# Kernel optimization log

Measured on AMD Instinct MI355X. Metric: run time of the kernel, lower is better.

Reference implementation:

```python
import jax, jax.numpy as jnp
import numpy as np
import math

B, L, DIM, H = 2, 2048, 512, 8


def setup_inputs() -> dict:
    key = jax.random.key(0)
    ks = jax.random.split(key, 8)
    s = 0.02
    return {
        "x": jax.random.normal(ks[0], (B, L, DIM), dtype=jnp.float32),
        "Wq": jax.random.normal(ks[1], (DIM, DIM), dtype=jnp.float32) * s,
        "Wk": jax.random.normal(ks[2], (DIM, DIM), dtype=jnp.float32) * s,
        "Wv": jax.random.normal(ks[3], (DIM, DIM), dtype=jnp.float32) * s,
        "Wb": jax.random.normal(ks[4], (H, DIM), dtype=jnp.float32) * s,   # content_bias weight
        "mixing": jax.random.normal(ks[5], (H, DIM), dtype=jnp.float32) * 0.2,  # UNIFORM init, std=0.2
        "Wd": jax.random.normal(ks[6], (DIM, DIM), dtype=jnp.float32) * s,
        "bd": jax.random.normal(ks[7], (DIM,), dtype=jnp.float32) * s,
    }


def reference(x, Wq, Wk, Wv, Wb, mixing, Wd, bd):
    b, l, d = x.shape
    h = mixing.shape[0]
    dh = d // h
    q = x @ Wq.T                      # [B,L,D]
    k = x @ Wk.T                      # [B,S,D]
    v = (x @ Wv.T).reshape(b, l, h, dh).transpose(0, 2, 1, 3)  # [B,H,S,dh]
    # scores[b,h,l,s] = sum_d q[b,l,d] * mixing[h,d] * k[b,s,d]
    scores = jnp.einsum("bld,hd,bsd->bhls", q, mixing, k)
    # content bias: [B,S,H] -> broadcast over query positions as [B,H,1,S]
    cb = jnp.einsum("bsd,hd->bhs", x, Wb)
    scale = math.sqrt(d / h)  # attention_head_size = dim / num_heads
    scores = (scores + cb[:, :, None, :]) / scale
    probs = jax.nn.softmax(scores, axis=-1)   # dropout disabled (eval)
    ctx = jnp.einsum("bhls,bhsd->bhld", probs, v)  # [B,H,L,dh]
    ctx = ctx.transpose(0, 2, 1, 3).reshape(b, l, d)
    return ctx @ Wd.T + bd
```

## Files before the change

kernel.cpp:

```cpp
#include <hip/hip_runtime.h>

#define B_ 2
#define L_ 2048
#define D_ 512
#define H_ 8
#define S_ 2048

typedef __attribute__((ext_vector_type(8))) short short8;
typedef __attribute__((ext_vector_type(8))) unsigned short ushort8;
typedef __attribute__((ext_vector_type(4))) unsigned short ushort4v;
typedef __attribute__((ext_vector_type(4))) float f32x4;
typedef __attribute__((ext_vector_type(16))) float f32x16;
typedef __attribute__((ext_vector_type(4))) float float4v;

__device__ __forceinline__ unsigned short f2bf(float f) {
    unsigned u = __float_as_uint(f);
    u += 0x7FFF + ((u >> 16) & 1);
    return (unsigned short)(u >> 16);
}
__device__ __forceinline__ float bf2f(unsigned short s) {
    return __uint_as_float(((unsigned)s) << 16);
}
__device__ __forceinline__ int swap23(int x) {
    return (x & ~12) | ((x & 4) << 1) | ((x & 8) >> 1);
}
__device__ __forceinline__ void async16(void* lds, const void* g) {
    __builtin_amdgcn_global_load_lds(
        (const __attribute__((address_space(1))) void*)(g),
        (__attribute__((address_space(3))) void*)(lds), 16, 0, 0);
}

__global__ __launch_bounds__(256) void cvt_all(const float* __restrict__ x,
                                               const float* __restrict__ w0, const float* __restrict__ w1,
                                               const float* __restrict__ w2, const float* __restrict__ w3,
                                               unsigned short* __restrict__ xb,
                                               unsigned short* __restrict__ d0, unsigned short* __restrict__ d1,
                                               unsigned short* __restrict__ d2, unsigned short* __restrict__ d3) {
    int i = blockIdx.x * 256 + threadIdx.x;
    const float* s;
    unsigned short* d;
    int idx;
    if (i < 524288) { s = x; d = xb; idx = i; }
    else {
        int off = i - 524288;
        int wsel = off >> 16; idx = off & 65535;
        s = (wsel == 0) ? w0 : (wsel == 1) ? w1 : (wsel == 2) ? w2 : w3;
        d = (wsel == 0) ? d0 : (wsel == 1) ? d1 : (wsel == 2) ? d2 : d3;
    }
    float4v v = *(const float4v*)(s + (size_t)idx * 4);
    ushort4v o;
    o[0] = f2bf(v[0]); o[1] = f2bf(v[1]); o[2] = f2bf(v[2]); o[3] = f2bf(v[3]);
    *(ushort4v*)(d + (size_t)idx * 4) = o;
}

__global__ __launch_bounds__(256) void cb_kernel(const float* __restrict__ x,
                                                 const float* __restrict__ Wb,
                                                 float* __restrict__ cb) {
    const int tid = threadIdx.x, w = tid >> 6, lane = tid & 63;
    const int row = blockIdx.x * 4 + w;
    const int h = lane >> 3, seg = lane & 7;
    const float* xp = x + (size_t)row * 512 + seg * 64;
    const float* wp = Wb + (size_t)h * 512 + seg * 64;
    float acc = 0.f;
    #pragma unroll
    for (int j = 0; j < 16; ++j) {
        float4v xv = *(const float4v*)(xp + j * 4);
        float4v wv = *(const float4v*)(wp + j * 4);
        acc += xv[0] * wv[0] + xv[1] * wv[1] + xv[2] * wv[2] + xv[3] * wv[3];
    }
    acc += __shfl_xor(acc, 1);
    acc += __shfl_xor(acc, 2);
    acc += __shfl_xor(acc, 4);
    if (seg == 0) {
        int b = row >> 11, s = row & 2047;
        cb[((size_t)(b * H_ + h)) * S_ + s] = acc * 0.125f;
    }
}

__device__ __forceinline__ void gemm128_core(const unsigned short* __restrict__ Ap,
                                             const unsigned short* __restrict__ Bp,
                                             short* sA, short* sB, int tid, f32x4 c[4][4]) {
    const int w = tid >> 6, lane = tid & 63, quad = lane >> 4, l15 = lane & 15;
    const int wm = (w >> 1) * 64, wn = (w & 1) * 64;
    for (int kc = 0; kc < 8; ++kc) {
        __syncthreads();
        #pragma unroll
        for (int j = 0; j < 4; ++j) {
            int i = tid + j * 256;
            int row = i >> 3, seg = i & 7;
            *(ushort8*)&sA[row * 72 + seg * 8] = *(const ushort8*)(Ap + (size_t)row * 512 + kc * 64 + seg * 8);
            *(ushort8*)&sB[row * 72 + seg * 8] = *(const ushort8*)(Bp + (size_t)row * 512 + kc * 64 + seg * 8);
        }
        __syncthreads();
        #pragma unroll
        for (int ks = 0; ks < 2; ++ks) {
            short8 a[4], b[4];
            #pragma unroll
            for (int ii = 0; ii < 4; ++ii)
                a[ii] = *(const short8*)&sA[(wm + ii * 16 + l15) * 72 + ks * 32 + quad * 8];
            #pragma unroll
            for (int jj = 0; jj < 4; ++jj)
                b[jj] = *(const short8*)&sB[(wn + jj * 16 + l15) * 72 + ks * 32 + quad * 8];
            #pragma unroll
            for (int ii = 0; ii < 4; ++ii)
                #pragma unroll
                for (int jj = 0; jj < 4; ++jj)
                    c[ii][jj] = __builtin_amdgcn_mfma_f32_16x16x32_bf16(a[ii], b[jj], c[ii][jj], 0, 0, 0);
        }
    }
}

__global__ __launch_bounds__(256) void gemm_qkv(const unsigned short* __restrict__ xb,
                                                const unsigned short* __restrict__ Wqb,
                                                const unsigned short* __restrict__ Wkb,
                                                const unsigned short* __restrict__ Wvb,
                                                unsigned short* __restrict__ qb,
                                                unsigned short* __restrict__ kpack,
                                                unsigned short* __restrict__ vt) {
    __shared__ short sA[128 * 72];
    __shared__ short sB[128 * 72];
    const int m0 = blockIdx.x * 128, n0 = blockIdx.y * 128, z = blockIdx.z;
    const unsigned short* Bsel = (z == 0) ? Wqb : ((z == 1) ? Wkb : Wvb);
    f32x4 c[4][4];
    #pragma unroll
    for (int ii = 0; ii < 4; ++ii)
        #pragma unroll
        for (int jj = 0; jj < 4; ++jj) { f32x4 zv = {0.f, 0.f, 0.f, 0.f}; c[ii][jj] = zv; }
    gemm128_core(xb + (size_t)m0 * 512, Bsel + (size_t)n0 * 512, sA, sB, threadIdx.x, c);
    const int tid = threadIdx.x, w = tid >> 6, lane = tid & 63, quad = lane >> 4, l15 = lane & 15;
    const int wm = (w >> 1) * 64, wn = (w & 1) * 64;
    #pragma unroll
    for (int ii = 0; ii < 4; ++ii) {
        const int mb = m0 + wm + ii * 16 + quad * 4;
        const int bb = mb >> 11;
        if (z == 0) {
            #pragma unroll
            for (int jj = 0; jj < 4; ++jj) {
                int ncol = n0 + wn + jj * 16 + l15;
                #pragma unroll
                for (int r = 0; r < 4; ++r)
                    qb[(size_t)(mb + r) * 512 + ncol] = f2bf(c[ii][jj][r]);
            }
        } else if (z == 1) {
            #pragma unroll
            for (int jj = 0; jj < 4; ++jj) {
                int d = n0 + wn + jj * 16 + l15;
                int f = d >> 4, hid = (d >> 3) & 1, jq = d & 7;
                #pragma unroll
                for (int r = 0; r < 4; ++r) {
                    int s = (mb + r) & 2047;
                    int t = s >> 5, rr = swap23(s & 31);
                    kpack[(((size_t)(bb * 64 + t)) * 32 + f) * 512 + hid * 256 + rr * 8 + jq]
                        = f2bf(c[ii][jj][r]);
                }
            }
        } else {
            const int hh = (n0 + wn) >> 6;
            const int s = mb & 2047;
            #pragma unroll
            for (int jj = 0; jj < 4; ++jj) {
                int dh = jj * 16 + l15;
                ushort4v o;
                o[0] = f2bf(c[ii][jj][0]); o[1] = f2bf(c[ii][jj][1]);
                o[2] = f2bf(c[ii][jj][2]); o[3] = f2bf(c[ii][jj][3]);
                *(ushort4v*)(vt + (((size_t)(bb * H_ + hh) * 64 + dh) * S_ + s)) = o;
            }
        }
    }
}

__global__ __launch_bounds__(256) void gemm_out(const unsigned short* __restrict__ ctxb,
                                                const unsigned short* __restrict__ Wdb,
                                                const float* __restrict__ bd,
                                                float* __restrict__ out) {
    __shared__ short sA[128 * 72];
    __shared__ short sB[128 * 72];
    const int m0 = blockIdx.x * 128, n0 = blockIdx.y * 128;
    f32x4 c[4][4];
    #pragma unroll
    for (int ii = 0; ii < 4; ++ii)
        #pragma unroll
        for (int jj = 0; jj < 4; ++jj) { f32x4 zv = {0.f, 0.f, 0.f, 0.f}; c[ii][jj] = zv; }
    gemm128_core(ctxb + (size_t)m0 * 512, Wdb + (size_t)n0 * 512, sA, sB, threadIdx.x, c);
    const int tid = threadIdx.x, w = tid >> 6, lane = tid & 63, quad = lane >> 4, l15 = lane & 15;
    const int wm = (w >> 1) * 64, wn = (w & 1) * 64;
    #pragma unroll
    for (int ii = 0; ii < 4; ++ii) {
        const int mb = m0 + wm + ii * 16 + quad * 4;
        #pragma unroll
        for (int jj = 0; jj < 4; ++jj) {
            int ncol = n0 + wn + jj * 16 + l15;
            float bias = bd[ncol];
            #pragma unroll
            for (int r = 0; r < 4; ++r)
                out[(size_t)(mb + r) * 512 + ncol] = c[ii][jj][r] + bias;
        }
    }
}

__global__ __launch_bounds__(256, 2) void flash_attn(const unsigned short* __restrict__ qb,
                                                     const unsigned short* __restrict__ kpack,
                                                     const unsigned short* __restrict__ vt,
                                                     const float* __restrict__ cb_all,
                                                     const float* __restrict__ mixing,
                                                     _Float16* __restrict__ Opart,
                                                     float* __restrict__ lpart) {
    __shared__ short sK[4][8192];
    __shared__ short sV[2][2048];
    const int bid = blockIdx.x;
    const int half = bid & 1, b = (bid >> 1) & 1, h = (bid >> 2) & 7, qt = bid >> 5;
    const int tid = threadIdx.x, w = tid >> 6, lane = tid & 63;
    const int l31 = lane & 31, hi = lane >> 5;
    const int q0 = qt * 128 + w * 32;
    const unsigned short* kbase = kpack + ((size_t)(b * 64 + half * 32)) * 32 * 512;
    const unsigned short* vtb = vt + ((size_t)(b * H_ + h) * 64) * (size_t)S_;
    const float* cbp = cb_all + (size_t)(b * H_ + h) * S_ + half * 1024;
    const float* mixh = mixing + h * D_;

    short8 qf[32];
    {
        const unsigned short* qrow = qb + ((size_t)(b * L_) + q0 + l31) * D_ + hi * 8;
        #pragma unroll
        for (int i = 0; i < 32; ++i) {
            ushort8 qv = *(const ushort8*)(qrow + i * 16);
            float4v ma = *(const float4v*)(mixh + i * 16 + hi * 8);
            float4v mb = *(const float4v*)(mixh + i * 16 + hi * 8 + 4);
            short8 ov;
            ov[0] = (short)f2bf(bf2f(qv[0]) * ma[0]);
            ov[1] = (short)f2bf(bf2f(qv[1]) * ma[1]);
            ov[2] = (short)f2bf(bf2f(qv[2]) * ma[2]);
            ov[3] = (short)f2bf(bf2f(qv[3]) * ma[3]);
            ov[4] = (short)f2bf(bf2f(qv[4]) * mb[0]);
            ov[5] = (short)f2bf(bf2f(qv[5]) * mb[1]);
            ov[6] = (short)f2bf(bf2f(qv[6]) * mb[2]);
            ov[7] = (short)f2bf(bf2f(qv[7]) * mb[3]);
            qf[i] = ov;
        }
    }
    asm volatile("s_waitcnt vmcnt(0)" ::: "memory");

    f32x16 acco0, acco1;
    #pragma unroll
    for (int i = 0; i < 16; ++i) { acco0[i] = 0.f; acco1[i] = 0.f; }
    float lsum = 0.f;
    f32x16 accsA, accsB;

    auto stageK = [&](int p) {
        const char* src = (const char*)(kbase + (size_t)p * 8192);
        char* dst = (char*)&sK[p & 3][0];
        #pragma unroll
        for (int ii = 0; ii < 4; ++ii)
            async16(dst + w * 1024 + ii * 4096, src + w * 1024 + ii * 4096 + (size_t)lane * 16);
    };
    auto stageV = [&](int u) {
        const unsigned short* gv = vtb + ((size_t)((w >> 1) * 32 + l31)) * (size_t)S_
                                   + half * 1024 + u * 32 + (w & 1) * 16 + hi * 8;
        async16((char*)&sV[u & 1][0] + w * 1024, gv);
    };
    auto qk_chunk = [&](const short* buf, int qbase) {
        __builtin_amdgcn_s_setprio(1);
        #pragma unroll
        for (int f = 0; f < 16; ++f) {
            short8 a = *(const short8*)&buf[f * 512 + lane * 8];
            if (f & 1) accsB = __builtin_amdgcn_mfma_f32_32x32x16_bf16(a, qf[qbase + f], accsB, 0, 0, 0);
            else       accsA = __builtin_amdgcn_mfma_f32_32x32x16_bf16(a, qf[qbase + f], accsA, 0, 0, 0);
        }
        __builtin_amdgcn_s_setprio(0);
    };
    auto softmax_pv = [&](int t) {
        const int s0 = t * 32;
        float p[16];
        #pragma unroll
        for (int R = 0; R < 16; ++R) {
            const int cr = (R & 3) + 8 * (R >> 2);
            const int idx = s0 + cr - 4 * ((R >> 2) & 1);
            float cbA = cbp[idx];
            float cbB = cbp[idx + 8];
            float cbv = hi ? cbB : cbA;
            float pe = __expf((accsA[R] + accsB[R]) * 0.125f + cbv);
            p[R] = pe;
            lsum += pe;
        }
        union { unsigned int u[4]; short8 s8; } P0, P1;
        #pragma unroll
        for (int j = 0; j < 4; ++j) {
            P0.u[j] = __builtin_amdgcn_perm(__float_as_uint(p[2 * j + 1]) + 0x8000u,
                                            __float_as_uint(p[2 * j]) + 0x8000u, 0x07060302u);
            P1.u[j] = __builtin_amdgcn_perm(__float_as_uint(p[8 + 2 * j + 1]) + 0x8000u,
                                            __float_as_uint(p[8 + 2 * j]) + 0x8000u, 0x07060302u);
        }
        const short* vbuf = &sV[t & 1][0];
        short8 av00 = *(const short8*)&vbuf[0 * 512 + lane * 8];
        short8 av01 = *(const short8*)&vbuf[1 * 512 + lane * 8];
        short8 av10 = *(const short8*)&vbuf[2 * 512 + lane * 8];
        short8 av11 = *(const short8*)&vbuf[3 * 512 + lane * 8];
        __builtin_amdgcn_s_setprio(1);
        acco0 = __builtin_amdgcn_mfma_f32_32x32x16_bf16(av00, P0.s8, acco0, 0, 0, 0);
        acco0 = __builtin_amdgcn_mfma_f32_32x32x16_bf16(av01, P1.s8, acco0, 0, 0, 0);
        acco1 = __builtin_amdgcn_mfma_f32_32x32x16_bf16(av10, P0.s8, acco1, 0, 0, 0);
        acco1 = __builtin_amdgcn_mfma_f32_32x32x16_bf16(av11, P1.s8, acco1, 0, 0, 0);
        __builtin_amdgcn_s_setprio(0);
    };

    stageK(0); stageK(1); stageV(0); stageK(2);

    for (int t = 0; t < 31; ++t) {
        #pragma unroll
        for (int i = 0; i < 16; ++i) { accsA[i] = 0.f; accsB[i] = 0.f; }
        const short* be = &sK[(t & 1) << 1][0];
        const short* bo = &sK[((t & 1) << 1) | 1][0];
        asm volatile("s_waitcnt vmcnt(9)" ::: "memory");
        __builtin_amdgcn_s_barrier();
        stageK(2 * t + 3);
        qk_chunk(be, 0);
        asm volatile("s_waitcnt vmcnt(8)" ::: "memory");
        __builtin_amdgcn_s_barrier();
        stageV(t + 1);
        if (t < 30) stageK(2 * t + 4);
        qk_chunk(bo, 16);
        softmax_pv(t);
    }
    {
        #pragma unroll
        for (int i = 0; i < 16; ++i) { accsA[i] = 0.f; accsB[i] = 0.f; }
        asm volatile("s_waitcnt vmcnt(5)" ::: "memory");
        __builtin_amdgcn_s_barrier();
        qk_chunk(&sK[2][0], 0);
        asm volatile("s_waitcnt vmcnt(0)" ::: "memory");
        __builtin_amdgcn_s_barrier();
        qk_chunk(&sK[3][0], 16);
        softmax_pv(31);
    }

    lsum += __shfl_xor(lsum, 32);
    if (hi == 0) lpart[(size_t)bid * 128 + w * 32 + l31] = lsum;
    #pragma unroll
    for (int R = 0; R < 16; ++R) {
        int dh = (R & 3) + 8 * (R >> 2) + 4 * hi;
        Opart[((size_t)bid * 64 + dh) * 128 + w * 32 + l31] = (_Float16)acco0[R];
        Opart[((size_t)bid * 64 + 32 + dh) * 128 + w * 32 + l31] = (_Float16)acco1[R];
    }
}

__global__ __launch_bounds__(256) void merge_ctx(const _Float16* __restrict__ Opart,
                                                 const float* __restrict__ lpart,
                                                 unsigned short* __restrict__ ctxb) {
    int t = blockIdx.x * 256 + threadIdx.x;
    int qq = t & 127, dh4 = (t >> 7) & 15, qt = (t >> 11) & 15, h = (t >> 15) & 7, b = t >> 18;
    int base = (qt << 5) | (h << 2) | (b << 1);
    float l = lpart[(size_t)base * 128 + qq] + lpart[(size_t)(base + 1) * 128 + qq];
    float inv = 1.f / l;
    ushort4v o;
    #pragma unroll
    for (int e = 0; e < 4; ++e) {
        int dh = dh4 * 4 + e;
        float v = (float)Opart[((size_t)base * 64 + dh) * 128 + qq]
                + (float)Opart[((size_t)(base + 1) * 64 + dh) * 128 + qq];
        o[e] = f2bf(v * inv);
    }
    *(ushort4v*)(ctxb + ((size_t)(b * L_) + qt * 128 + qq) * 512 + h * 64 + dh4 * 4) = o;
}

extern "C" void kernel_launch(void* const* d_in, const int* in_sizes, int n_in,
                              void* d_out, int out_size, void* d_ws, size_t ws_size,
                              hipStream_t stream) {
    (void)in_sizes; (void)n_in; (void)out_size; (void)ws_size;
    const float* x      = (const float*)d_in[0];
    const float* Wq     = (const float*)d_in[1];
    const float* Wk     = (const float*)d_in[2];
    const float* Wv     = (const float*)d_in[3];
    const float* Wb     = (const float*)d_in[4];
    const float* mixing = (const float*)d_in[5];
    const float* Wd     = (const float*)d_in[6];
    const float* bd     = (const float*)d_in[7];
    float* out = (float*)d_out;

    char* ws = (char*)d_ws;
    const size_t MiB = 1048576;
    unsigned short* xb    = (unsigned short*)(ws);
    unsigned short* qb    = (unsigned short*)(ws + 4 * MiB);
    unsigned short* kpack = (unsigned short*)(ws + 8 * MiB);
    unsigned short* vt    = (unsigned short*)(ws + 12 * MiB);
    unsigned short* ctxb  = (unsigned short*)(ws + 16 * MiB);
    unsigned short* Wqb   = (unsigned short*)(ws + 20 * MiB);
    unsigned short* Wkb   = (unsigned short*)(ws + 20 * MiB + 512 * 1024);
    unsigned short* Wvb   = (unsigned short*)(ws + 21 * MiB);
    unsigned short* Wdb   = (unsigned short*)(ws + 21 * MiB + 512 * 1024);
    float* cbuf           = (float*)(ws + 22 * MiB);
    float* lpart          = (float*)(ws + 23 * MiB);
    _Float16* Opart       = (_Float16*)(ws + 24 * MiB);

    cvt_all<<<3072, 256, 0, stream>>>(x, Wq, Wk, Wv, Wd, xb, Wqb, Wkb, Wvb, Wdb);
    gemm_qkv<<<dim3(32, 4, 3), 256, 0, stream>>>(xb, Wqb, Wkb, Wvb, qb, kpack, vt);
    cb_kernel<<<1024, 256, 0, stream>>>(x, Wb, cbuf);
    flash_attn<<<512, 256, 0, stream>>>(qb, kpack, vt, cbuf, mixing, Opart, lpart);
    merge_ctx<<<2048, 256, 0, stream>>>(Opart, lpart, ctxb);
    gemm_out<<<dim3(32, 4), 256, 0, stream>>>(ctxb, Wdb, bd, out);
}
```

Measured before the change: 210.7 us.

## Process two 32-row query tiles per wave to reuse staged K/V

Each wave now handles 64 query rows instead of 32, reusing every K and V fragment loaded from shared memory for two MFMA streams. The grid is halved to 256 blocks, launch bounds drop to one block per SM, and the merge kernel indexing is updated to the wider tiles. The aim is to halve K/V global and LDS traffic per query. The cost is doubled register use for Q fragments and accumulators, lower occupancy, and fewer blocks than a 256-CU device can fully balance.

New measurement: 270.9 us. 28.6% more time.

```diff
diff --git a/kernel.cpp b/kernel.cpp
--- a/kernel.cpp
+++ b/kernel.cpp
@@ -198,7 +198,7 @@
     }
 }
 
-__global__ __launch_bounds__(256, 2) void flash_attn(const unsigned short* __restrict__ qb,
+__global__ __launch_bounds__(256, 1) void flash_attn(const unsigned short* __restrict__ qb,
                                                      const unsigned short* __restrict__ kpack,
                                                      const unsigned short* __restrict__ vt,
                                                      const float* __restrict__ cb_all,
@@ -211,15 +211,16 @@
     const int half = bid & 1, b = (bid >> 1) & 1, h = (bid >> 2) & 7, qt = bid >> 5;
     const int tid = threadIdx.x, w = tid >> 6, lane = tid & 63;
     const int l31 = lane & 31, hi = lane >> 5;
-    const int q0 = qt * 128 + w * 32;
+    const int q0 = qt * 256 + w * 64;
     const unsigned short* kbase = kpack + ((size_t)(b * 64 + half * 32)) * 32 * 512;
     const unsigned short* vtb = vt + ((size_t)(b * H_ + h) * 64) * (size_t)S_;
     const float* cbp = cb_all + (size_t)(b * H_ + h) * S_ + half * 1024;
     const float* mixh = mixing + h * D_;
 
-    short8 qf[32];
-    {
-        const unsigned short* qrow = qb + ((size_t)(b * L_) + q0 + l31) * D_ + hi * 8;
+    short8 qf0[32], qf1[32];
+    #pragma unroll
+    for (int qb2 = 0; qb2 < 2; ++qb2) {
+        const unsigned short* qrow = qb + ((size_t)(b * L_) + q0 + qb2 * 32 + l31) * D_ + hi * 8;
         #pragma unroll
         for (int i = 0; i < 32; ++i) {
             ushort8 qv = *(const ushort8*)(qrow + i * 16);
@@ -234,16 +235,16 @@
             ov[5] = (short)f2bf(bf2f(qv[5]) * mb[1]);
             ov[6] = (short)f2bf(bf2f(qv[6]) * mb[2]);
             ov[7] = (short)f2bf(bf2f(qv[7]) * mb[3]);
-            qf[i] = ov;
+            if (qb2) qf1[i] = ov; else qf0[i] = ov;
         }
     }
     asm volatile("s_waitcnt vmcnt(0)" ::: "memory");
 
-    f32x16 acco0, acco1;
-    #pragma unroll
-    for (int i = 0; i < 16; ++i) { acco0[i] = 0.f; acco1[i] = 0.f; }
-    float lsum = 0.f;
-    f32x16 accsA, accsB;
+    f32x16 accoA0, accoB0, accoA1, accoB1;
+    #pragma unroll
+    for (int i = 0; i < 16; ++i) { accoA0[i] = 0.f; accoB0[i] = 0.f; accoA1[i] = 0.f; accoB1[i] = 0.f; }
+    float lsum0 = 0.f, lsum1 = 0.f;
+    f32x16 accs0, accs1;
 
     auto stageK = [&](int p) {
         const char* src = (const char*)(kbase + (size_t)p * 8192);
@@ -262,14 +263,14 @@
         #pragma unroll
         for (int f = 0; f < 16; ++f) {
             short8 a = *(const short8*)&buf[f * 512 + lane * 8];
-            if (f & 1) accsB = __builtin_amdgcn_mfma_f32_32x32x16_bf16(a, qf[qbase + f], accsB, 0, 0, 0);
-            else       accsA = __builtin_amdgcn_mfma_f32_32x32x16_bf16(a, qf[qbase + f], accsA, 0, 0, 0);
+            accs0 = __builtin_amdgcn_mfma_f32_32x32x16_bf16(a, qf0[qbase + f], accs0, 0, 0, 0);
+            accs1 = __builtin_amdgcn_mfma_f32_32x32x16_bf16(a, qf1[qbase + f], accs1, 0, 0, 0);
         }
         __builtin_amdgcn_s_setprio(0);
     };
     auto softmax_pv = [&](int t) {
         const int s0 = t * 32;
-        float p[16];
+        float p0[16], p1[16];
         #pragma unroll
         for (int R = 0; R < 16; ++R) {
             const int cr = (R & 3) + 8 * (R >> 2);
@@ -277,36 +278,46 @@
             float cbA = cbp[idx];
             float cbB = cbp[idx + 8];
             float cbv = hi ? cbB : cbA;
-            float pe = __expf((accsA[R] + accsB[R]) * 0.125f + cbv);
-            p[R] = pe;
-            lsum += pe;
-        }
-        union { unsigned int u[4]; short8 s8; } P0, P1;
+            float pe0 = __expf(accs0[R] * 0.125f + cbv);
+            float pe1 = __expf(accs1[R] * 0.125f + cbv);
+            p0[R] = pe0; lsum0 += pe0;
+            p1[R] = pe1; lsum1 += pe1;
+        }
+        union { unsigned int u[4]; short8 s8; } Pa0, Pb0, Pa1, Pb1;
         #pragma unroll
         for (int j = 0; j < 4; ++j) {
-            P0.u[j] = __builtin_amdgcn_perm(__float_as_uint(p[2 * j + 1]) + 0x8000u,
-                                            __float_as_uint(p[2 * j]) + 0x8000u, 0x07060302u);
-            P1.u[j] = __builtin_amdgcn_perm(__float_as_uint(p[8 + 2 * j + 1]) + 0x8000u,
-                                            __float_as_uint(p[8 + 2 * j]) + 0x8000u, 0x07060302u);
-        }
-        const short* vbuf = &sV[t & 1][0];
-        short8 av00 = *(const short8*)&vbuf[0 * 512 + lane * 8];
-        short8 av01 = *(const short8*)&vbuf[1 * 512 + lane * 8];
-        short8 av10 = *(const short8*)&vbuf[2 * 512 + lane * 8];
-        short8 av11 = *(const short8*)&vbuf[3 * 512 + lane * 8];
-        __builtin_amdgcn_s_setprio(1);
-        acco0 = __builtin_amdgcn_mfma_f32_32x32x16_bf16(av00, P0.s8, acco0, 0, 0, 0);
-        acco0 = __builtin_amdgcn_mfma_f32_32x32x16_bf16(av01, P1.s8, acco0, 0, 0, 0);
-        acco1 = __builtin_amdgcn_mfma_f32_32x32x16_bf16(av10, P0.s8, acco1, 0, 0, 0);
-        acco1 = __builtin_amdgcn_mfma_f32_32x32x16_bf16(av11, P1.s8, acco1, 0, 0, 0);
-        __builtin_amdgcn_s_setprio(0);
+            Pa0.u[j] = __builtin_amdgcn_perm(__float_as_uint(p0[2 * j + 1]) + 0x8000u,
+                                             __float_as_uint(p0[2 * j]) + 0x8000u, 0x07060302u);
+            Pb0.u[j] = __builtin_amdgcn_perm(__float_as_uint(p0[8 + 2 * j + 1]) + 0x8000u,
+                                             __float_as_uint(p0[8 + 2 * j]) + 0x8000u, 0x07060302u);
+            Pa1.u[j] = __builtin_amdgcn_perm(__float_as_uint(p1[2 * j + 1]) + 0x8000u,
+                                             __float_as_uint(p1[2 * j]) + 0x8000u, 0x07060302u);
+            Pb1.u[j] = __builtin_amdgcn_perm(__float_as_uint(p1[8 + 2 * j + 1]) + 0x8000u,
+                                             __float_as_uint(p1[8 + 2 * j]) + 0x8000u, 0x07060302u);
+        }
+        {
+            short8 av00 = *(const short8*)&sV[t & 1][0 * 512 + lane * 8];
+            short8 av01 = *(const short8*)&sV[t & 1][1 * 512 + lane * 8];
+            short8 av10 = *(const short8*)&sV[t & 1][2 * 512 + lane * 8];
+            short8 av11 = *(const short8*)&sV[t & 1][3 * 512 + lane * 8];
+            __builtin_amdgcn_s_setprio(1);
+            accoA0 = __builtin_amdgcn_mfma_f32_32x32x16_bf16(av00, Pa0.s8, accoA0, 0, 0, 0);
+            accoB0 = __builtin_amdgcn_mfma_f32_32x32x16_bf16(av10, Pa0.s8, accoB0, 0, 0, 0);
+            accoA1 = __builtin_amdgcn_mfma_f32_32x32x16_bf16(av00, Pa1.s8, accoA1, 0, 0, 0);
+            accoB1 = __builtin_amdgcn_mfma_f32_32x32x16_bf16(av10, Pa1.s8, accoB1, 0, 0, 0);
+            accoA0 = __builtin_amdgcn_mfma_f32_32x32x16_bf16(av01, Pb0.s8, accoA0, 0, 0, 0);
+            accoB0 = __builtin_amdgcn_mfma_f32_32x32x16_bf16(av11, Pb0.s8, accoB0, 0, 0, 0);
+            accoA1 = __builtin_amdgcn_mfma_f32_32x32x16_bf16(av01, Pb1.s8, accoA1, 0, 0, 0);
+            accoB1 = __builtin_amdgcn_mfma_f32_32x32x16_bf16(av11, Pb1.s8, accoB1, 0, 0, 0);
+            __builtin_amdgcn_s_setprio(0);
+        }
     };
 
-    stageK(0); stageK(1); stageV(0); stageK(2);
+    stageK(0); stageV(0); stageK(1); stageK(2);
 
     for (int t = 0; t < 31; ++t) {
         #pragma unroll
-        for (int i = 0; i < 16; ++i) { accsA[i] = 0.f; accsB[i] = 0.f; }
+        for (int i = 0; i < 16; ++i) { accs0[i] = 0.f; accs1[i] = 0.f; }
         const short* be = &sK[(t & 1) << 1][0];
         const short* bo = &sK[((t & 1) << 1) | 1][0];
         asm volatile("s_waitcnt vmcnt(9)" ::: "memory");
@@ -322,7 +333,7 @@
     }
     {
         #pragma unroll
-        for (int i = 0; i < 16; ++i) { accsA[i] = 0.f; accsB[i] = 0.f; }
+        for (int i = 0; i < 16; ++i) { accs0[i] = 0.f; accs1[i] = 0.f; }
         asm volatile("s_waitcnt vmcnt(5)" ::: "memory");
         __builtin_amdgcn_s_barrier();
         qk_chunk(&sK[2][0], 0);
@@ -332,13 +343,19 @@
         softmax_pv(31);
     }
 
-    lsum += __shfl_xor(lsum, 32);
-    if (hi == 0) lpart[(size_t)bid * 128 + w * 32 + l31] = lsum;
+    lsum0 += __shfl_xor(lsum0, 32);
+    lsum1 += __shfl_xor(lsum1, 32);
+    if (hi == 0) {
+        lpart[(size_t)bid * 256 + w * 64 + l31] = lsum0;
+        lpart[(size_t)bid * 256 + w * 64 + 32 + l31] = lsum1;
+    }
     #pragma unroll
     for (int R = 0; R < 16; ++R) {
         int dh = (R & 3) + 8 * (R >> 2) + 4 * hi;
-        Opart[((size_t)bid * 64 + dh) * 128 + w * 32 + l31] = (_Float16)acco0[R];
-        Opart[((size_t)bid * 64 + 32 + dh) * 128 + w * 32 + l31] = (_Float16)acco1[R];
+        Opart[((size_t)bid * 64 + dh) * 256 + w * 64 + l31] = (_Float16)accoA0[R];
+        Opart[((size_t)bid * 64 + 32 + dh) * 256 + w * 64 + l31] = (_Float16)accoB0[R];
+        Opart[((size_t)bid * 64 + dh) * 256 + w * 64 + 32 + l31] = (_Float16)accoA1[R];
+        Opart[((size_t)bid * 64 + 32 + dh) * 256 + w * 64 + 32 + l31] = (_Float16)accoB1[R];
     }
 }
 
@@ -346,19 +363,19 @@
                                                  const float* __restrict__ lpart,
                                                  unsigned short* __restrict__ ctxb) {
     int t = blockIdx.x * 256 + threadIdx.x;
-    int qq = t & 127, dh4 = (t >> 7) & 15, qt = (t >> 11) & 15, h = (t >> 15) & 7, b = t >> 18;
+    int qq = t & 255, dh4 = (t >> 8) & 15, qt = (t >> 12) & 7, h = (t >> 15) & 7, b = t >> 18;
     int base = (qt << 5) | (h << 2) | (b << 1);
-    float l = lpart[(size_t)base * 128 + qq] + lpart[(size_t)(base + 1) * 128 + qq];
+    float l = lpart[(size_t)base * 256 + qq] + lpart[(size_t)(base + 1) * 256 + qq];
     float inv = 1.f / l;
     ushort4v o;
     #pragma unroll
     for (int e = 0; e < 4; ++e) {
         int dh = dh4 * 4 + e;
-        float v = (float)Opart[((size_t)base * 64 + dh) * 128 + qq]
-                + (float)Opart[((size_t)(base + 1) * 64 + dh) * 128 + qq];
+        float v = (float)Opart[((size_t)base * 64 + dh) * 256 + qq]
+                + (float)Opart[((size_t)(base + 1) * 64 + dh) * 256 + qq];
         o[e] = f2bf(v * inv);
     }
-    *(ushort4v*)(ctxb + ((size_t)(b * L_) + qt * 128 + qq) * 512 + h * 64 + dh4 * 4) = o;
+    *(ushort4v*)(ctxb + ((size_t)(b * L_) + qt * 256 + qq) * 512 + h * 64 + dh4 * 4) = o;
 }
 
 extern "C" void kernel_launch(void* const* d_in, const int* in_sizes, int n_in,
@@ -393,7 +410,7 @@
     cvt_all<<<3072, 256, 0, stream>>>(x, Wq, Wk, Wv, Wd, xb, Wqb, Wkb, Wvb, Wdb);
     gemm_qkv<<<dim3(32, 4, 3), 256, 0, stream>>>(xb, Wqb, Wkb, Wvb, qb, kpack, vt);
     cb_kernel<<<1024, 256, 0, stream>>>(x, Wb, cbuf);
-    flash_attn<<<512, 256, 0, stream>>>(qb, kpack, vt, cbuf, mixing, Opart, lpart);
+    flash_attn<<<256, 256, 0, stream>>>(qb, kpack, vt, cbuf, mixing, Opart, lpart);
     merge_ctx<<<2048, 256, 0, stream>>>(Opart, lpart, ctxb);
     gemm_out<<<dim3(32, 4), 256, 0, stream>>>(ctxb, Wdb, bd, out);
 }
```

## Pre-swizzle V into MFMA fragment layout and load it directly to registers

Applied to the files above, without the earlier changes.

The QKV GEMM epilogue now writes V in a fragment-ordered layout, so each flash-attention lane can load its PV operand straight from global memory into registers. This removes the LDS staging buffer for V and its async copies, and the vmcnt waits are recounted to match. The conversion kernel and the content-bias kernel are also merged into one launch to cut a kernel boundary. The cost is register pressure from holding V operands across the QK compute, and V latency now sits directly on the softmax/PV path.

After: 217.6 us. +3.3%, slower.

```diff
diff --git a/kernel.cpp b/kernel.cpp
--- a/kernel.cpp
+++ b/kernel.cpp
@@ -30,50 +30,50 @@
         (__attribute__((address_space(3))) void*)(lds), 16, 0, 0);
 }
 
-__global__ __launch_bounds__(256) void cvt_all(const float* __restrict__ x,
-                                               const float* __restrict__ w0, const float* __restrict__ w1,
-                                               const float* __restrict__ w2, const float* __restrict__ w3,
-                                               unsigned short* __restrict__ xb,
-                                               unsigned short* __restrict__ d0, unsigned short* __restrict__ d1,
-                                               unsigned short* __restrict__ d2, unsigned short* __restrict__ d3) {
-    int i = blockIdx.x * 256 + threadIdx.x;
-    const float* s;
-    unsigned short* d;
-    int idx;
-    if (i < 524288) { s = x; d = xb; idx = i; }
-    else {
-        int off = i - 524288;
-        int wsel = off >> 16; idx = off & 65535;
-        s = (wsel == 0) ? w0 : (wsel == 1) ? w1 : (wsel == 2) ? w2 : w3;
-        d = (wsel == 0) ? d0 : (wsel == 1) ? d1 : (wsel == 2) ? d2 : d3;
-    }
-    float4v v = *(const float4v*)(s + (size_t)idx * 4);
-    ushort4v o;
-    o[0] = f2bf(v[0]); o[1] = f2bf(v[1]); o[2] = f2bf(v[2]); o[3] = f2bf(v[3]);
-    *(ushort4v*)(d + (size_t)idx * 4) = o;
-}
-
-__global__ __launch_bounds__(256) void cb_kernel(const float* __restrict__ x,
-                                                 const float* __restrict__ Wb,
-                                                 float* __restrict__ cb) {
-    const int tid = threadIdx.x, w = tid >> 6, lane = tid & 63;
-    const int row = blockIdx.x * 4 + w;
-    const int h = lane >> 3, seg = lane & 7;
-    const float* xp = x + (size_t)row * 512 + seg * 64;
-    const float* wp = Wb + (size_t)h * 512 + seg * 64;
-    float acc = 0.f;
-    #pragma unroll
-    for (int j = 0; j < 16; ++j) {
-        float4v xv = *(const float4v*)(xp + j * 4);
-        float4v wv = *(const float4v*)(wp + j * 4);
-        acc += xv[0] * wv[0] + xv[1] * wv[1] + xv[2] * wv[2] + xv[3] * wv[3];
-    }
-    acc += __shfl_xor(acc, 1);
-    acc += __shfl_xor(acc, 2);
-    acc += __shfl_xor(acc, 4);
-    if (seg == 0) {
-        int b = row >> 11, s = row & 2047;
-        cb[((size_t)(b * H_ + h)) * S_ + s] = acc * 0.125f;
+__global__ __launch_bounds__(256) void cvt_cb(const float* __restrict__ x,
+                                              const float* __restrict__ w0, const float* __restrict__ w1,
+                                              const float* __restrict__ w2, const float* __restrict__ w3,
+                                              const float* __restrict__ Wb,
+                                              unsigned short* __restrict__ xb,
+                                              unsigned short* __restrict__ d0, unsigned short* __restrict__ d1,
+                                              unsigned short* __restrict__ d2, unsigned short* __restrict__ d3,
+                                              float* __restrict__ cb) {
+    if (blockIdx.x < 3072) {
+        int i = blockIdx.x * 256 + threadIdx.x;
+        const float* s;
+        unsigned short* d;
+        int idx;
+        if (i < 524288) { s = x; d = xb; idx = i; }
+        else {
+            int off = i - 524288;
+            int wsel = off >> 16; idx = off & 65535;
+            s = (wsel == 0) ? w0 : (wsel == 1) ? w1 : (wsel == 2) ? w2 : w3;
+            d = (wsel == 0) ? d0 : (wsel == 1) ? d1 : (wsel == 2) ? d2 : d3;
+        }
+        float4v v = *(const float4v*)(s + (size_t)idx * 4);
+        ushort4v o;
+        o[0] = f2bf(v[0]); o[1] = f2bf(v[1]); o[2] = f2bf(v[2]); o[3] = f2bf(v[3]);
+        *(ushort4v*)(d + (size_t)idx * 4) = o;
+    } else {
+        const int tid = threadIdx.x, w = tid >> 6, lane = tid & 63;
+        const int row = (blockIdx.x - 3072) * 4 + w;
+        const int h = lane >> 3, seg = lane & 7;
+        const float* xp = x + (size_t)row * 512 + seg * 64;
+        const float* wp = Wb + (size_t)h * 512 + seg * 64;
+        float acc = 0.f;
+        #pragma unroll
+        for (int j = 0; j < 16; ++j) {
+            float4v xv = *(const float4v*)(xp + j * 4);
+            float4v wv = *(const float4v*)(wp + j * 4);
+            acc += xv[0] * wv[0] + xv[1] * wv[1] + xv[2] * wv[2] + xv[3] * wv[3];
+        }
+        acc += __shfl_xor(acc, 1);
+        acc += __shfl_xor(acc, 2);
+        acc += __shfl_xor(acc, 4);
+        if (seg == 0) {
+            int b = row >> 11, s = row & 2047;
+            cb[((size_t)(b * H_ + h)) * S_ + s] = acc * 0.125f;
+        }
     }
 }
 
@@ -116,7 +116,7 @@
                                                 const unsigned short* __restrict__ Wvb,
                                                 unsigned short* __restrict__ qb,
                                                 unsigned short* __restrict__ kpack,
-                                                unsigned short* __restrict__ vt) {
+                                                unsigned short* __restrict__ vfrag) {
     __shared__ short sA[128 * 72];
     __shared__ short sB[128 * 72];
     const int m0 = blockIdx.x * 128, n0 = blockIdx.y * 128, z = blockIdx.z;
@@ -163,7 +163,9 @@
                 ushort4v o;
                 o[0] = f2bf(c[ii][jj][0]); o[1] = f2bf(c[ii][jj][1]);
                 o[2] = f2bf(c[ii][jj][2]); o[3] = f2bf(c[ii][jj][3]);
-                *(ushort4v*)(vt + (((size_t)(bb * H_ + hh) * 64 + dh) * S_ + s)) = o;
+                size_t blk = ((size_t)(bb * H_ + hh) * 64 + (s >> 5)) * 4
+                           + ((dh >> 5) * 2 + ((s >> 4) & 1));
+                *(ushort4v*)(vfrag + blk * 512 + (dh & 31) * 8 + ((s >> 3) & 1) * 256 + (s & 7)) = o;
             }
         }
     }
@@ -200,20 +202,19 @@
 
 __global__ __launch_bounds__(256, 2) void flash_attn(const unsigned short* __restrict__ qb,
                                                      const unsigned short* __restrict__ kpack,
-                                                     const unsigned short* __restrict__ vt,
+                                                     const unsigned short* __restrict__ vfrag,
                                                      const float* __restrict__ cb_all,
                                                      const float* __restrict__ mixing,
                                                      _Float16* __restrict__ Opart,
                                                      float* __restrict__ lpart) {
     __shared__ short sK[4][8192];
-    __shared__ short sV[2][2048];
     const int bid = blockIdx.x;
     const int half = bid & 1, b = (bid >> 1) & 1, h = (bid >> 2) & 7, qt = bid >> 5;
     const int tid = threadIdx.x, w = tid >> 6, lane = tid & 63;
     const int l31 = lane & 31, hi = lane >> 5;
     const int q0 = qt * 128 + w * 32;
     const unsigned short* kbase = kpack + ((size_t)(b * 64 + half * 32)) * 32 * 512;
-    const unsigned short* vtb = vt + ((size_t)(b * H_ + h) * 64) * (size_t)S_;
+    const unsigned short* vfb = vfrag + ((size_t)(b * H_ + h) * 64 + half * 32) * 2048;
     const float* cbp = cb_all + (size_t)(b * H_ + h) * S_ + half * 1024;
     const float* mixh = mixing + h * D_;
 
@@ -244,6 +245,7 @@
     for (int i = 0; i < 16; ++i) { acco0[i] = 0.f; acco1[i] = 0.f; }
     float lsum = 0.f;
     f32x16 accsA, accsB;
+    short8 av00, av01, av10, av11;
 
     auto stageK = [&](int p) {
         const char* src = (const char*)(kbase + (size_t)p * 8192);
@@ -252,10 +254,13 @@
         for (int ii = 0; ii < 4; ++ii)
             async16(dst + w * 1024 + ii * 4096, src + w * 1024 + ii * 4096 + (size_t)lane * 16);
     };
-    auto stageV = [&](int u) {
-        const unsigned short* gv = vtb + ((size_t)((w >> 1) * 32 + l31)) * (size_t)S_
-                                   + half * 1024 + u * 32 + (w & 1) * 16 + hi * 8;
-        async16((char*)&sV[u & 1][0] + w * 1024, gv);
+    auto ldV = [&](int t) {
+        const unsigned short* vp = vfb + (size_t)t * 2048 + lane * 8;
+        av00 = *(const short8*)(vp);
+        av01 = *(const short8*)(vp + 512);
+        av10 = *(const short8*)(vp + 1024);
+        av11 = *(const short8*)(vp + 1536);
+        asm volatile("" ::: "memory");
     };
     auto qk_chunk = [&](const short* buf, int qbase) {
         __builtin_amdgcn_s_setprio(1);
@@ -289,11 +294,6 @@
             P1.u[j] = __builtin_amdgcn_perm(__float_as_uint(p[8 + 2 * j + 1]) + 0x8000u,
                                             __float_as_uint(p[8 + 2 * j]) + 0x8000u, 0x07060302u);
         }
-        const short* vbuf = &sV[t & 1][0];
-        short8 av00 = *(const short8*)&vbuf[0 * 512 + lane * 8];
-        short8 av01 = *(const short8*)&vbuf[1 * 512 + lane * 8];
-        short8 av10 = *(const short8*)&vbuf[2 * 512 + lane * 8];
-        short8 av11 = *(const short8*)&vbuf[3 * 512 + lane * 8];
         __builtin_amdgcn_s_setprio(1);
         acco0 = __builtin_amdgcn_mfma_f32_32x32x16_bf16(av00, P0.s8, acco0, 0, 0, 0);
         acco0 = __builtin_amdgcn_mfma_f32_32x32x16_bf16(av01, P1.s8, acco0, 0, 0, 0);
@@ -302,33 +302,36 @@
         __builtin_amdgcn_s_setprio(0);
     };
 
-    stageK(0); stageK(1); stageV(0); stageK(2);
+    stageK(0); stageK(1); stageK(2);
 
     for (int t = 0; t < 31; ++t) {
         #pragma unroll
         for (int i = 0; i < 16; ++i) { accsA[i] = 0.f; accsB[i] = 0.f; }
         const short* be = &sK[(t & 1) << 1][0];
         const short* bo = &sK[((t & 1) << 1) | 1][0];
-        asm volatile("s_waitcnt vmcnt(9)" ::: "memory");
+        asm volatile("s_waitcnt vmcnt(8)" ::: "memory");
         __builtin_amdgcn_s_barrier();
+        ldV(t);
         stageK(2 * t + 3);
         qk_chunk(be, 0);
+        asm volatile("s_waitcnt vmcnt(12)" ::: "memory");
+        __builtin_amdgcn_s_barrier();
+        if (t < 30) stageK(2 * t + 4);
+        qk_chunk(bo, 16);
+        asm volatile("s_waitcnt vmcnt(8)" ::: "memory");
+        softmax_pv(t);
+    }
+    {
+        #pragma unroll
+        for (int i = 0; i < 16; ++i) { accsA[i] = 0.f; accsB[i] = 0.f; }
         asm volatile("s_waitcnt vmcnt(8)" ::: "memory");
         __builtin_amdgcn_s_barrier();
-        stageV(t + 1);
-        if (t < 30) stageK(2 * t + 4);
-        qk_chunk(bo, 16);
-        softmax_pv(t);
-    }
-    {
-        #pragma unroll
-        for (int i = 0; i < 16; ++i) { accsA[i] = 0.f; accsB[i] = 0.f; }
-        asm volatile("s_waitcnt vmcnt(5)" ::: "memory");
-        __builtin_amdgcn_s_barrier();
+        ldV(31);
         qk_chunk(&sK[2][0], 0);
-        asm volatile("s_waitcnt vmcnt(0)" ::: "memory");
+        asm volatile("s_waitcnt vmcnt(4)" ::: "memory");
         __builtin_amdgcn_s_barrier();
         qk_chunk(&sK[3][0], 16);
+        asm volatile("s_waitcnt vmcnt(0)" ::: "memory");
         softmax_pv(31);
     }
 
@@ -380,7 +383,7 @@
     unsigned short* xb    = (unsigned short*)(ws);
     unsigned short* qb    = (unsigned short*)(ws + 4 * MiB);
     unsigned short* kpack = (unsigned short*)(ws + 8 * MiB);
-    unsigned short* vt    = (unsigned short*)(ws + 12 * MiB);
+    unsigned short* vfrag = (unsigned short*)(ws + 12 * MiB);
     unsigned short* ctxb  = (unsigned short*)(ws + 16 * MiB);
     unsigned short* Wqb   = (unsigned short*)(ws + 20 * MiB);
     unsigned short* Wkb   = (unsigned short*)(ws + 20 * MiB + 512 * 1024);
@@ -390,10 +393,9 @@
     float* lpart          = (float*)(ws + 23 * MiB);
     _Float16* Opart       = (_Float16*)(ws + 24 * MiB);
 
-    cvt_all<<<3072, 256, 0, stream>>>(x, Wq, Wk, Wv, Wd, xb, Wqb, Wkb, Wvb, Wdb);
-    gemm_qkv<<<dim3(32, 4, 3), 256, 0, stream>>>(xb, Wqb, Wkb, Wvb, qb, kpack, vt);
-    cb_kernel<<<1024, 256, 0, stream>>>(x, Wb, cbuf);
-    flash_attn<<<512, 256, 0, stream>>>(qb, kpack, vt, cbuf, mixing, Opart, lpart);
+    cvt_cb<<<4096, 256, 0, stream>>>(x, Wq, Wk, Wv, Wd, Wb, xb, Wqb, Wkb, Wvb, Wdb, cbuf);
+    gemm_qkv<<<dim3(32, 4, 3), 256, 0, stream>>>(xb, Wqb, Wkb, Wvb, qb, kpack, vfrag);
+    flash_attn<<<512, 256, 0, stream>>>(qb, kpack, vfrag, cbuf, mixing, Opart, lpart);
     merge_ctx<<<2048, 256, 0, stream>>>(Opart, lpart, ctxb);
     gemm_out<<<dim3(32, 4), 256, 0, stream>>>(ctxb, Wdb, bd, out);
 }
```
